# Kernel optimization log

Hardware: AMD Instinct MI355X
Metric: run time of the kernel (lower is better)

The kernel has to match this reference:

```python
import jax, jax.numpy as jnp
import numpy as np

EPS = 1e-6
D_CONV = 4

def _layernorm(x):
    m = jnp.mean(x, axis=-1, keepdims=True)
    v = jnp.mean((x - m) ** 2, axis=-1, keepdims=True)
    return (x - m) / jnp.sqrt(v + EPS)

def setup_inputs() -> dict:
    key = jax.random.key(0)
    ks = jax.random.split(key, 20)
    B, L, D = 2, 4096, 1024
    Di = D          # expand = 1
    N = 16          # d_state
    R = 64          # dt_rank = ceil(D/16)
    H = 4 * D       # mlp hidden
    s = 0.02
    rn = lambda k, sh: s * jax.random.normal(k, sh, dtype=jnp.float32)
    x = jax.random.normal(ks[0], (B, L, D), dtype=jnp.float32)
    path = jax.random.permutation(ks[1], L).astype(jnp.int32)
    path_rev = jnp.argsort(path).astype(jnp.int32)
    A_log = jnp.log(jnp.tile(jnp.arange(1, N + 1, dtype=jnp.float32)[None, :], (Di, 1)))
    return {
        'x': x, 'path': path, 'path_rev': path_rev,
        'in_proj_w': rn(ks[2], (2 * Di, D)),
        'conv_w': rn(ks[3], (Di, D_CONV)), 'conv_b': rn(ks[4], (Di,)),
        'x_proj_w': rn(ks[5], (R + 2 * N, Di)),
        'dt_proj_w': rn(ks[6], (Di, R)), 'dt_proj_b': rn(ks[7], (Di,)),
        'A_log': A_log, 'D_param': jnp.ones((Di,), dtype=jnp.float32),
        'out_proj_w': rn(ks[8], (D, Di)),
        'fc1_w': rn(ks[9], (H, D)), 'fc1_b': jnp.zeros((H,), dtype=jnp.float32),
        'fc2_w': rn(ks[10], (D, H)), 'fc2_b': jnp.zeros((D,), dtype=jnp.float32),
    }

def _mamba(u, in_proj_w, conv_w, conv_b, x_proj_w, dt_proj_w, dt_proj_b, A_log, D_param, out_proj_w):
    B, L, _ = u.shape
    N = A_log.shape[1]
    R = dt_proj_w.shape[1]
    xz = u @ in_proj_w.T                      # (B,L,2*Di)
    xi, z = jnp.split(xz, 2, axis=-1)
    # causal depthwise conv1d, kernel 4
    xpad = jnp.pad(xi, ((0, 0), (D_CONV - 1, 0), (0, 0)))
    xc = conv_b + sum(conv_w[:, k] * xpad[:, k:k + L, :] for k in range(D_CONV))
    xc = jax.nn.silu(xc)                      # (B,L,Di)
    proj = xc @ x_proj_w.T                    # (B,L,R+2N)
    dt_r = proj[..., :R]
    Bm = proj[..., R:R + N]                   # (B,L,N)
    Cm = proj[..., R + N:]                    # (B,L,N)
    dt = jax.nn.softplus(dt_r @ dt_proj_w.T + dt_proj_b)  # (B,L,Di)
    A = -jnp.exp(A_log)                       # (Di,N)

    def step(h, inp):
        dt_t, B_t, C_t, x_t = inp             # (B,Di),(B,N),(B,N),(B,Di)
        dA = jnp.exp(dt_t[:, :, None] * A)    # (B,Di,N)
        h = dA * h + (dt_t * x_t)[:, :, None] * B_t[:, None, :]
        y = jnp.einsum('bdn,bn->bd', h, C_t)
        return h, y

    h0 = jnp.zeros((B, xc.shape[-1], N), dtype=u.dtype)
    xs = (dt.transpose(1, 0, 2), Bm.transpose(1, 0, 2), Cm.transpose(1, 0, 2), xc.transpose(1, 0, 2))
    _, ys = jax.lax.scan(step, h0, xs)        # (L,B,Di)
    y = ys.transpose(1, 0, 2) + D_param * xc
    y = y * jax.nn.silu(z)
    return y @ out_proj_w.T

def reference(x, path, path_rev, in_proj_w, conv_w, conv_b, x_proj_w, dt_proj_w, dt_proj_b,
              A_log, D_param, out_proj_w, fc1_w, fc1_b, fc2_w, fc2_b):
    tmp1 = x[:, path, :]                      # zigzag gather
    tmp1 = _mamba(_layernorm(tmp1), in_proj_w, conv_w, conv_b, x_proj_w,
                  dt_proj_w, dt_proj_b, A_log, D_param, out_proj_w)
    x = x + tmp1[:, path_rev, :]              # zigzag scatter (inverse gather)
    h = _layernorm(x)
    h = jax.nn.gelu(h @ fc1_w.T + fc1_b, approximate=True) @ fc2_w.T + fc2_b
    return x + h
```

## Files before the change

### kernel.cpp

```cpp
#include <hip/hip_runtime.h>
#include <cstdint>
#include <cstddef>

typedef unsigned short u16;
typedef __bf16 bf16x8 __attribute__((ext_vector_type(8)));
typedef float f32x4 __attribute__((ext_vector_type(4)));

#define B_ 2
#define L_ 4096
#define D_ 1024
#define N_ 16
#define BL_ 8192
#define NC_ 64
#define LC_ 64

__device__ __forceinline__ float bf2f(u16 h) {
  union { unsigned int u; float f; } v; v.u = ((unsigned int)h) << 16; return v.f;
}
__device__ __forceinline__ u16 f2bf(float f) {
  union { float f; unsigned int u; } v; v.f = f;
  unsigned int r = v.u + 0x7FFFu + ((v.u >> 16) & 1u);
  return (u16)(r >> 16);
}
__device__ __forceinline__ float sigmoidf_(float x) { return 1.0f / (1.0f + __expf(-x)); }

#define WBF_TOT 11730944
__global__ __launch_bounds__(256) void cvt_w_k(
    const float* __restrict__ s0, const float* __restrict__ s1,
    const float* __restrict__ s2, const float* __restrict__ s3,
    const float* __restrict__ s4, const float* __restrict__ s5,
    u16* __restrict__ dst)
{
  int i = blockIdx.x * 256 + threadIdx.x;
  if (i >= WBF_TOT) return;
  float v;
  if (i < 2097152) v = s0[i];
  else if (i < 2228224) { int j = i - 2097152; v = (j < 98304) ? s1[j] : 0.0f; }
  else if (i < 2293760) v = s2[i - 2228224];
  else if (i < 3342336) v = s3[i - 2293760];
  else if (i < 7536640) v = s4[i - 3342336];
  else v = s5[i - 7536640];
  dst[i] = f2bf(v);
}

#define BM 128
#define BN 128
#define BK 32

enum { M_NONE = 0, M_PROJ = 1, M_SOFTPLUS = 2, M_GELU = 3, M_BIASRES = 4 };

template<int MODE>
__global__ __launch_bounds__(256) void gemm_bt(
    const u16* __restrict__ A, const u16* __restrict__ W,
    float* __restrict__ C, u16* __restrict__ C2,
    const float* __restrict__ bias, const float* __restrict__ resid,
    int M, int N, int K)
{
  __shared__ __align__(16) u16 As[BM * BK];
  __shared__ __align__(16) u16 Bs[BN * BK];
  const int bm = blockIdx.y * BM;
  const int bn = blockIdx.x * BN;
  const int tid = threadIdx.x;
  const int lane = tid & 63;
  const int wave = tid >> 6;
  const int wr = (wave >> 1) * 64;
  const int wc = (wave & 1) * 64;

  f32x4 acc[4][4];
#pragma unroll
  for (int i = 0; i < 4; ++i)
#pragma unroll
    for (int j = 0; j < 4; ++j)
#pragma unroll
      for (int r = 0; r < 4; ++r) acc[i][j][r] = 0.0f;

  const int r0 = tid >> 2;
  const int r1 = (tid + 256) >> 2;
  const int ke = (tid & 3) << 3;

  for (int k0 = 0; k0 < K; k0 += BK) {
    __builtin_amdgcn_global_load_lds(
        (const __attribute__((address_space(1))) void*)(A + (size_t)(bm + r0) * K + k0 + ke),
        (__attribute__((address_space(3))) void*)(&As[(size_t)tid * 8]), 16, 0, 0);
    __builtin_amdgcn_global_load_lds(
        (const __attribute__((address_space(1))) void*)(A + (size_t)(bm + r1) * K + k0 + ke),
        (__attribute__((address_space(3))) void*)(&As[(size_t)(tid + 256) * 8]), 16, 0, 0);
    __builtin_amdgcn_global_load_lds(
        (const __attribute__((address_space(1))) void*)(W + (size_t)(bn + r0) * K + k0 + ke),
        (__attribute__((address_space(3))) void*)(&Bs[(size_t)tid * 8]), 16, 0, 0);
    __builtin_amdgcn_global_load_lds(
        (const __attribute__((address_space(1))) void*)(W + (size_t)(bn + r1) * K + k0 + ke),
        (__attribute__((address_space(3))) void*)(&Bs[(size_t)(tid + 256) * 8]), 16, 0, 0);
    __syncthreads();
    const int kq = (lane >> 4) << 3;
    const int mr = lane & 15;
    bf16x8 af[4], bfr[4];
#pragma unroll
    for (int i = 0; i < 4; ++i)
      af[i] = *(const bf16x8*)(&As[(wr + i * 16 + mr) * BK + kq]);
#pragma unroll
    for (int j = 0; j < 4; ++j)
      bfr[j] = *(const bf16x8*)(&Bs[(wc + j * 16 + mr) * BK + kq]);
#pragma unroll
    for (int i = 0; i < 4; ++i)
#pragma unroll
      for (int j = 0; j < 4; ++j)
        acc[i][j] = __builtin_amdgcn_mfma_f32_16x16x32_bf16(af[i], bfr[j], acc[i][j], 0, 0, 0);
    __syncthreads();
  }

  const int mlo = (lane >> 4) << 2;
  const int nlo = lane & 15;
#pragma unroll
  for (int i = 0; i < 4; ++i) {
#pragma unroll
    for (int j = 0; j < 4; ++j) {
      int col = bn + wc + j * 16 + nlo;
      if (col < N) {
#pragma unroll
        for (int r = 0; r < 4; ++r) {
          int row = bm + wr + i * 16 + mlo + r;
          float v = acc[i][j][r];
          if constexpr (MODE == M_NONE) {
            C[(size_t)row * N + col] = v;
          } else if constexpr (MODE == M_PROJ) {
            C[(size_t)row * N + col] = v;
            if (col < 64) C2[((size_t)row << 6) + col] = f2bf(v);
          } else if constexpr (MODE == M_SOFTPLUS) {
            v += bias[col];
            C[(size_t)row * N + col] = (v > 20.0f) ? v : log1pf(__expf(v));
          } else if constexpr (MODE == M_GELU) {
            v += bias[col];
            float a = 0.7978845608028654f * (v + 0.044715f * v * v * v);
            float t = 1.0f - 2.0f / (__expf(2.0f * a) + 1.0f);
            C2[(size_t)row * N + col] = f2bf(0.5f * v * (1.0f + t));
          } else if constexpr (MODE == M_BIASRES) {
            C[(size_t)row * N + col] = v + bias[col] + resid[(size_t)row * N + col];
          }
        }
      }
    }
  }
}

__device__ __forceinline__ void blockReduce2(float& s, float& q) {
#pragma unroll
  for (int o = 32; o > 0; o >>= 1) { s += __shfl_down(s, o, 64); q += __shfl_down(q, o, 64); }
  __shared__ float red[2][4];
  int lane = threadIdx.x & 63, wave = threadIdx.x >> 6;
  if (lane == 0) { red[0][wave] = s; red[1][wave] = q; }
  __syncthreads();
  s = red[0][0] + red[0][1] + red[0][2] + red[0][3];
  q = red[1][0] + red[1][1] + red[1][2] + red[1][3];
}

__global__ __launch_bounds__(256) void ln_gather_k(
    const float* __restrict__ x, const int* __restrict__ path, u16* __restrict__ out)
{
  int b = blockIdx.x >> 12;
  int l = blockIdx.x & 4095;
  int src = path[l];
  const float* row = x + (((size_t)b * L_ + src) << 10);
  u16* orow = out + (((size_t)b * L_ + l) << 10);
  float v[4], s = 0.f, q = 0.f;
#pragma unroll
  for (int i = 0; i < 4; ++i) {
    v[i] = row[threadIdx.x + (i << 8)];
    s += v[i]; q += v[i] * v[i];
  }
  blockReduce2(s, q);
  float mean = s * (1.0f / 1024.0f);
  float var = q * (1.0f / 1024.0f) - mean * mean;
  float rstd = rsqrtf(var + 1e-6f);
#pragma unroll
  for (int i = 0; i < 4; ++i)
    orow[threadIdx.x + (i << 8)] = f2bf((v[i] - mean) * rstd);
}

__global__ __launch_bounds__(256) void ln_scatter_k(
    const float* __restrict__ x, const int* __restrict__ prev,
    const float* __restrict__ mo, float* __restrict__ xnew, u16* __restrict__ lnout)
{
  int b = blockIdx.x >> 12;
  int l = blockIdx.x & 4095;
  int pl = prev[l];
  const float* xr = x + (((size_t)b * L_ + l) << 10);
  const float* mr_ = mo + (((size_t)b * L_ + pl) << 10);
  size_t base = ((size_t)blockIdx.x) << 10;
  float v[4], s = 0.f, q = 0.f;
#pragma unroll
  for (int i = 0; i < 4; ++i) {
    v[i] = xr[threadIdx.x + (i << 8)] + mr_[threadIdx.x + (i << 8)];
    s += v[i]; q += v[i] * v[i];
  }
  blockReduce2(s, q);
  float mean = s * (1.0f / 1024.0f);
  float var = q * (1.0f / 1024.0f) - mean * mean;
  float rstd = rsqrtf(var + 1e-6f);
#pragma unroll
  for (int i = 0; i < 4; ++i) {
    xnew[base + threadIdx.x + (i << 8)] = v[i];
    lnout[base + threadIdx.x + (i << 8)] = f2bf((v[i] - mean) * rstd);
  }
}

__global__ __launch_bounds__(256) void conv_silu_k(
    const float* __restrict__ xz, const float* __restrict__ cw, const float* __restrict__ cb,
    u16* __restrict__ xc)
{
  int idx = blockIdx.x * 256 + threadIdx.x;
  int d = idx & 1023;
  int l = (idx >> 10) & 4095;
  int b = idx >> 22;
  float acc = cb[d];
#pragma unroll
  for (int k = 0; k < 4; ++k) {
    int ls = l + k - 3;
    if (ls >= 0)
      acc += cw[(d << 2) + k] * xz[(((size_t)b * L_ + ls) << 11) + d];
  }
  acc = acc * sigmoidf_(acc);
  xc[idx] = f2bf(acc);
}

__global__ __launch_bounds__(256) void scan_p1_k(
    const float* __restrict__ dt, const u16* __restrict__ xc, const float* __restrict__ proj,
    const float* __restrict__ A_log, float* __restrict__ acum, float* __restrict__ hloc)
{
  int c = blockIdx.x & (NC_ - 1);
  int q = (blockIdx.x >> 6) & 3;
  int b = blockIdx.x >> 8;
  int d = (q << 8) + threadIdx.x;
  float Arow[N_];
#pragma unroll
  for (int n = 0; n < N_; ++n) Arow[n] = -__expf(A_log[(d << 4) + n]);
  float h[N_], ac[N_];
#pragma unroll
  for (int n = 0; n < N_; ++n) { h[n] = 0.0f; ac[n] = 1.0f; }
  int l0 = c << 6;
  for (int i = 0; i < LC_; ++i) {
    size_t rowb = (size_t)b * L_ + (l0 + i);
    float dtv = dt[(rowb << 10) + d];
    float xv = bf2f(xc[(rowb << 10) + d]);
    float dtx = dtv * xv;
    const float* Bp = proj + rowb * 96 + 64;
#pragma unroll
    for (int n = 0; n < N_; ++n) {
      float dA = __expf(dtv * Arow[n]);
      h[n] = dA * h[n] + dtx * Bp[n];
      ac[n] *= dA;
    }
  }
  size_t sb = ((((size_t)b << 10) + d) << 10) + (c << 4);
#pragma unroll
  for (int n = 0; n < N_; ++n) { acum[sb + n] = ac[n]; hloc[sb + n] = h[n]; }
}

__global__ __launch_bounds__(256) void scan_p2_k(
    const float* __restrict__ acum, const float* __restrict__ hloc, float* __restrict__ hin)
{
  int idx = blockIdx.x * 256 + threadIdx.x;
  int n = idx & 15;
  int dn = idx >> 4;
  size_t base = ((size_t)dn << 10) + n;
  float hs = 0.0f;
  for (int c = 0; c < NC_; ++c) {
    hin[base + (c << 4)] = hs;
    hs = acum[base + (c << 4)] * hs + hloc[base + (c << 4)];
  }
}

__global__ __launch_bounds__(256) void scan_p3_k(
    const float* __restrict__ dt, const u16* __restrict__ xc, const float* __restrict__ proj,
    const float* __restrict__ A_log, const float* __restrict__ Dp, const float* __restrict__ hin,
    const float* __restrict__ xz, u16* __restrict__ yg)
{
  int c = blockIdx.x & (NC_ - 1);
  int q = (blockIdx.x >> 6) & 3;
  int b = blockIdx.x >> 8;
  int d = (q << 8) + threadIdx.x;
  float Arow[N_];
#pragma unroll
  for (int n = 0; n < N_; ++n) Arow[n] = -__expf(A_log[(d << 4) + n]);
  float h[N_];
  size_t sb = ((((size_t)b << 10) + d) << 10) + (c << 4);
#pragma unroll
  for (int n = 0; n < N_; ++n) h[n] = hin[sb + n];
  float Dv = Dp[d];
  int l0 = c << 6;
  for (int i = 0; i < LC_; ++i) {
    size_t rowb = (size_t)b * L_ + (l0 + i);
    float dtv = dt[(rowb << 10) + d];
    float xv = bf2f(xc[(rowb << 10) + d]);
    float dtx = dtv * xv;
    const float* Bp = proj + rowb * 96 + 64;
    const float* Cp = proj + rowb * 96 + 80;
    float y = 0.0f;
#pragma unroll
    for (int n = 0; n < N_; ++n) {
      float dA = __expf(dtv * Arow[n]);
      h[n] = dA * h[n] + dtx * Bp[n];
      y += h[n] * Cp[n];
    }
    y += Dv * xv;
    float zv = xz[(rowb << 11) + 1024 + d];
    yg[(rowb << 10) + d] = f2bf(y * zv * sigmoidf_(zv));
  }
}

extern "C" void kernel_launch(void* const* d_in, const int* in_sizes, int n_in,
                              void* d_out, int out_size, void* d_ws, size_t ws_size,
                              hipStream_t stream)
{
  const float* x_in      = (const float*)d_in[0];
  const int*   path      = (const int*)d_in[1];
  const int*   path_rev  = (const int*)d_in[2];
  const float* in_proj_w = (const float*)d_in[3];
  const float* conv_w    = (const float*)d_in[4];
  const float* conv_b    = (const float*)d_in[5];
  const float* x_proj_w  = (const float*)d_in[6];
  const float* dt_proj_w = (const float*)d_in[7];
  const float* dt_proj_b = (const float*)d_in[8];
  const float* A_log     = (const float*)d_in[9];
  const float* Dp        = (const float*)d_in[10];
  const float* out_pw    = (const float*)d_in[11];
  const float* fc1_w     = (const float*)d_in[12];
  const float* fc1_b     = (const float*)d_in[13];
  const float* fc2_w     = (const float*)d_in[14];
  const float* fc2_b     = (const float*)d_in[15];
  float* out = (float*)d_out;

  char* w = (char*)d_ws;
  size_t off = 0;
  auto alloc = [&](size_t bytes) -> char* {
    char* p = w + off;
    off = (off + bytes + 255) & ~(size_t)255;
    return p;
  };
  u16*   wbf   = (u16*)  alloc((size_t)WBF_TOT * 2);
  u16*   ln_bf = (u16*)  alloc((size_t)BL_ * 1024 * 2);
  float* xz    = (float*)alloc((size_t)BL_ * 2048 * 4);
  u16*   xc    = (u16*)  alloc((size_t)BL_ * 1024 * 2);
  char*  pool0 = alloc(0);
  float* proj  = (float*)alloc((size_t)BL_ * 96 * 4);
  u16*   dtr   = (u16*)  alloc((size_t)BL_ * 64 * 2);
  float* dt    = (float*)alloc((size_t)BL_ * 1024 * 4);
  float* acum  = (float*)alloc((size_t)2 * 1024 * NC_ * 16 * 4);
  float* hloc  = (float*)alloc((size_t)2 * 1024 * NC_ * 16 * 4);
  float* hin   = (float*)alloc((size_t)2 * 1024 * NC_ * 16 * 4);
  u16*   yg    = (u16*)  alloc((size_t)BL_ * 1024 * 2);
  float* mo    = xz;
  float* xnew  = (float*)((char*)xz + (size_t)BL_ * 1024 * 4);
  u16*   h1b   = (u16*)pool0;

  const u16* w_inp = wbf;
  const u16* w_xp  = wbf + 2097152;
  const u16* w_dtp = wbf + 2228224;
  const u16* w_op  = wbf + 2293760;
  const u16* w_fc1 = wbf + 3342336;
  const u16* w_fc2 = wbf + 7536640;

  dim3 blk(256);
  cvt_w_k<<<WBF_TOT / 256, blk, 0, stream>>>(in_proj_w, x_proj_w, dt_proj_w, out_pw,
                                             fc1_w, fc2_w, wbf);
  ln_gather_k<<<BL_, blk, 0, stream>>>(x_in, path, ln_bf);
  gemm_bt<M_NONE><<<dim3(16, 64), blk, 0, stream>>>(ln_bf, w_inp, xz, nullptr, nullptr, nullptr, 8192, 2048, 1024);
  conv_silu_k<<<(BL_ * 1024) / 256, blk, 0, stream>>>(xz, conv_w, conv_b, xc);
  gemm_bt<M_PROJ><<<dim3(1, 64), blk, 0, stream>>>(xc, w_xp, proj, dtr, nullptr, nullptr, 8192, 96, 1024);
  gemm_bt<M_SOFTPLUS><<<dim3(8, 64), blk, 0, stream>>>(dtr, w_dtp, dt, nullptr, dt_proj_b, nullptr, 8192, 1024, 64);
  scan_p1_k<<<2 * 4 * NC_, blk, 0, stream>>>(dt, xc, proj, A_log, acum, hloc);
  scan_p2_k<<<(2 * 1024 * 16) / 256, blk, 0, stream>>>(acum, hloc, hin);
  scan_p3_k<<<2 * 4 * NC_, blk, 0, stream>>>(dt, xc, proj, A_log, Dp, hin, xz, yg);
  gemm_bt<M_NONE><<<dim3(8, 64), blk, 0, stream>>>(yg, w_op, mo, nullptr, nullptr, nullptr, 8192, 1024, 1024);
  ln_scatter_k<<<BL_, blk, 0, stream>>>(x_in, path_rev, mo, xnew, ln_bf);
  gemm_bt<M_GELU><<<dim3(32, 64), blk, 0, stream>>>(ln_bf, w_fc1, nullptr, h1b, fc1_b, nullptr, 8192, 4096, 1024);
  gemm_bt<M_BIASRES><<<dim3(8, 64), blk, 0, stream>>>(h1b, w_fc2, out, nullptr, fc2_b, xnew, 8192, 1024, 4096);
}
```

Measured before the change: 682.1 us.

## Double-buffer GEMM LDS tiles, remap blocks per XCD, store xz/mo in bf16

The GEMM now double-buffers its A/B LDS tiles, issuing the next k-slice's global-to-LDS loads before computing the current one. This drops one barrier per iteration and overlaps load latency with MFMA work. Block IDs are remapped so each XCD handles a contiguous band of M rows, aiming for better L2 reuse. The in_proj and out_proj outputs (xz and mo) are written as bf16 instead of fp32, halving that traffic at some cost in precision; xnew gets its own allocation.

```diff
diff --git a/kernel.cpp b/kernel.cpp
--- a/kernel.cpp
+++ b/kernel.cpp
@@ -47,7 +47,11 @@
 #define BN 128
 #define BK 32
 
-enum { M_NONE = 0, M_PROJ = 1, M_SOFTPLUS = 2, M_GELU = 3, M_BIASRES = 4 };
+enum { M_BF16 = 0, M_PROJ = 1, M_SOFTPLUS = 2, M_GELU = 3, M_BIASRES = 4 };
+
+#define GLDS(gp, lp) __builtin_amdgcn_global_load_lds( \
+    (const __attribute__((address_space(1))) void*)(gp), \
+    (__attribute__((address_space(3))) void*)(lp), 16, 0, 0)
 
 template<int MODE>
 __global__ __launch_bounds__(256) void gemm_bt(
@@ -56,10 +60,18 @@
     const float* __restrict__ bias, const float* __restrict__ resid,
     int M, int N, int K)
 {
-  __shared__ __align__(16) u16 As[BM * BK];
-  __shared__ __align__(16) u16 Bs[BN * BK];
-  const int bm = blockIdx.y * BM;
-  const int bn = blockIdx.x * BN;
+  __shared__ __align__(16) u16 As[2][BM * BK];
+  __shared__ __align__(16) u16 Bs[2][BN * BK];
+
+  const int id = blockIdx.x + gridDim.x * blockIdx.y;
+  const int xcd = id & 7;
+  const int q = id >> 3;
+  const int bandH = gridDim.y >> 3;
+  const int xs = q % gridDim.x;
+  const int ys = xcd * bandH + q / gridDim.x;
+  const int bm = ys * BM;
+  const int bn = xs * BN;
+
   const int tid = threadIdx.x;
   const int lane = tid & 63;
   const int wave = tid >> 6;
@@ -75,38 +87,38 @@
       for (int r = 0; r < 4; ++r) acc[i][j][r] = 0.0f;
 
   const int r0 = tid >> 2;
-  const int r1 = (tid + 256) >> 2;
   const int ke = (tid & 3) << 3;
-
+  const u16* Ab = A + (size_t)(bm + r0) * K + ke;
+  const u16* Wb = W + (size_t)(bn + r0) * K + ke;
+  const size_t rstep = (size_t)64 * K;
+
+  auto issue = [&](int buf, int k0) {
+    GLDS(Ab + k0, &As[buf][tid * 8]);
+    GLDS(Ab + k0 + rstep, &As[buf][(tid + 256) * 8]);
+    GLDS(Wb + k0, &Bs[buf][tid * 8]);
+    GLDS(Wb + k0 + rstep, &Bs[buf][(tid + 256) * 8]);
+  };
+
+  issue(0, 0);
+  int cur = 0;
+  const int kq = (lane >> 4) << 3;
+  const int mr = lane & 15;
   for (int k0 = 0; k0 < K; k0 += BK) {
-    __builtin_amdgcn_global_load_lds(
-        (const __attribute__((address_space(1))) void*)(A + (size_t)(bm + r0) * K + k0 + ke),
-        (__attribute__((address_space(3))) void*)(&As[(size_t)tid * 8]), 16, 0, 0);
-    __builtin_amdgcn_global_load_lds(
-        (const __attribute__((address_space(1))) void*)(A + (size_t)(bm + r1) * K + k0 + ke),
-        (__attribute__((address_space(3))) void*)(&As[(size_t)(tid + 256) * 8]), 16, 0, 0);
-    __builtin_amdgcn_global_load_lds(
-        (const __attribute__((address_space(1))) void*)(W + (size_t)(bn + r0) * K + k0 + ke),
-        (__attribute__((address_space(3))) void*)(&Bs[(size_t)tid * 8]), 16, 0, 0);
-    __builtin_amdgcn_global_load_lds(
-        (const __attribute__((address_space(1))) void*)(W + (size_t)(bn + r1) * K + k0 + ke),
-        (__attribute__((address_space(3))) void*)(&Bs[(size_t)(tid + 256) * 8]), 16, 0, 0);
     __syncthreads();
-    const int kq = (lane >> 4) << 3;
-    const int mr = lane & 15;
+    if (k0 + BK < K) issue(cur ^ 1, k0 + BK);
     bf16x8 af[4], bfr[4];
 #pragma unroll
     for (int i = 0; i < 4; ++i)
-      af[i] = *(const bf16x8*)(&As[(wr + i * 16 + mr) * BK + kq]);
+      af[i] = *(const bf16x8*)(&As[cur][(wr + i * 16 + mr) * BK + kq]);
 #pragma unroll
     for (int j = 0; j < 4; ++j)
-      bfr[j] = *(const bf16x8*)(&Bs[(wc + j * 16 + mr) * BK + kq]);
+      bfr[j] = *(const bf16x8*)(&Bs[cur][(wc + j * 16 + mr) * BK + kq]);
 #pragma unroll
     for (int i = 0; i < 4; ++i)
 #pragma unroll
       for (int j = 0; j < 4; ++j)
         acc[i][j] = __builtin_amdgcn_mfma_f32_16x16x32_bf16(af[i], bfr[j], acc[i][j], 0, 0, 0);
-    __syncthreads();
+    cur ^= 1;
   }
 
   const int mlo = (lane >> 4) << 2;
@@ -121,10 +133,10 @@
         for (int r = 0; r < 4; ++r) {
           int row = bm + wr + i * 16 + mlo + r;
           float v = acc[i][j][r];
-          if constexpr (MODE == M_NONE) {
-            C[(size_t)row * N + col] = v;
+          if constexpr (MODE == M_BF16) {
+            C2[(size_t)row * N + col] = f2bf(v);
           } else if constexpr (MODE == M_PROJ) {
-            C[(size_t)row * N + col] = v;
+            C[(size_t)row * 96 + col] = v;
             if (col < 64) C2[((size_t)row << 6) + col] = f2bf(v);
           } else if constexpr (MODE == M_SOFTPLUS) {
             v += bias[col];
@@ -179,18 +191,18 @@
 
 __global__ __launch_bounds__(256) void ln_scatter_k(
     const float* __restrict__ x, const int* __restrict__ prev,
-    const float* __restrict__ mo, float* __restrict__ xnew, u16* __restrict__ lnout)
+    const u16* __restrict__ mo, float* __restrict__ xnew, u16* __restrict__ lnout)
 {
   int b = blockIdx.x >> 12;
   int l = blockIdx.x & 4095;
   int pl = prev[l];
   const float* xr = x + (((size_t)b * L_ + l) << 10);
-  const float* mr_ = mo + (((size_t)b * L_ + pl) << 10);
+  const u16* mr_ = mo + (((size_t)b * L_ + pl) << 10);
   size_t base = ((size_t)blockIdx.x) << 10;
   float v[4], s = 0.f, q = 0.f;
 #pragma unroll
   for (int i = 0; i < 4; ++i) {
-    v[i] = xr[threadIdx.x + (i << 8)] + mr_[threadIdx.x + (i << 8)];
+    v[i] = xr[threadIdx.x + (i << 8)] + bf2f(mr_[threadIdx.x + (i << 8)]);
     s += v[i]; q += v[i] * v[i];
   }
   blockReduce2(s, q);
@@ -205,7 +217,7 @@
 }
 
 __global__ __launch_bounds__(256) void conv_silu_k(
-    const float* __restrict__ xz, const float* __restrict__ cw, const float* __restrict__ cb,
+    const u16* __restrict__ xz, const float* __restrict__ cw, const float* __restrict__ cb,
     u16* __restrict__ xc)
 {
   int idx = blockIdx.x * 256 + threadIdx.x;
@@ -217,7 +229,7 @@
   for (int k = 0; k < 4; ++k) {
     int ls = l + k - 3;
     if (ls >= 0)
-      acc += cw[(d << 2) + k] * xz[(((size_t)b * L_ + ls) << 11) + d];
+      acc += cw[(d << 2) + k] * bf2f(xz[(((size_t)b * L_ + ls) << 11) + d]);
   }
   acc = acc * sigmoidf_(acc);
   xc[idx] = f2bf(acc);
@@ -273,7 +285,7 @@
 __global__ __launch_bounds__(256) void scan_p3_k(
     const float* __restrict__ dt, const u16* __restrict__ xc, const float* __restrict__ proj,
     const float* __restrict__ A_log, const float* __restrict__ Dp, const float* __restrict__ hin,
-    const float* __restrict__ xz, u16* __restrict__ yg)
+    const u16* __restrict__ xz, u16* __restrict__ yg)
 {
   int c = blockIdx.x & (NC_ - 1);
   int q = (blockIdx.x >> 6) & 3;
@@ -303,7 +315,7 @@
       y += h[n] * Cp[n];
     }
     y += Dv * xv;
-    float zv = xz[(rowb << 11) + 1024 + d];
+    float zv = bf2f(xz[(rowb << 11) + 1024 + d]);
     yg[(rowb << 10) + d] = f2bf(y * zv * sigmoidf_(zv));
   }
 }
@@ -339,7 +351,7 @@
   };
   u16*   wbf   = (u16*)  alloc((size_t)WBF_TOT * 2);
   u16*   ln_bf = (u16*)  alloc((size_t)BL_ * 1024 * 2);
-  float* xz    = (float*)alloc((size_t)BL_ * 2048 * 4);
+  u16*   xz    = (u16*)  alloc((size_t)BL_ * 2048 * 2);
   u16*   xc    = (u16*)  alloc((size_t)BL_ * 1024 * 2);
   char*  pool0 = alloc(0);
   float* proj  = (float*)alloc((size_t)BL_ * 96 * 4);
@@ -349,8 +361,8 @@
   float* hloc  = (float*)alloc((size_t)2 * 1024 * NC_ * 16 * 4);
   float* hin   = (float*)alloc((size_t)2 * 1024 * NC_ * 16 * 4);
   u16*   yg    = (u16*)  alloc((size_t)BL_ * 1024 * 2);
-  float* mo    = xz;
-  float* xnew  = (float*)((char*)xz + (size_t)BL_ * 1024 * 4);
+  float* xnew  = (float*)alloc((size_t)BL_ * 1024 * 4);
+  u16*   mo    = xz;
   u16*   h1b   = (u16*)pool0;
 
   const u16* w_inp = wbf;
@@ -364,14 +376,14 @@
   cvt_w_k<<<WBF_TOT / 256, blk, 0, stream>>>(in_proj_w, x_proj_w, dt_proj_w, out_pw,
                                              fc1_w, fc2_w, wbf);
   ln_gather_k<<<BL_, blk, 0, stream>>>(x_in, path, ln_bf);
-  gemm_bt<M_NONE><<<dim3(16, 64), blk, 0, stream>>>(ln_bf, w_inp, xz, nullptr, nullptr, nullptr, 8192, 2048, 1024);
+  gemm_bt<M_BF16><<<dim3(16, 64), blk, 0, stream>>>(ln_bf, w_inp, nullptr, xz, nullptr, nullptr, 8192, 2048, 1024);
   conv_silu_k<<<(BL_ * 1024) / 256, blk, 0, stream>>>(xz, conv_w, conv_b, xc);
   gemm_bt<M_PROJ><<<dim3(1, 64), blk, 0, stream>>>(xc, w_xp, proj, dtr, nullptr, nullptr, 8192, 96, 1024);
   gemm_bt<M_SOFTPLUS><<<dim3(8, 64), blk, 0, stream>>>(dtr, w_dtp, dt, nullptr, dt_proj_b, nullptr, 8192, 1024, 64);
   scan_p1_k<<<2 * 4 * NC_, blk, 0, stream>>>(dt, xc, proj, A_log, acum, hloc);
   scan_p2_k<<<(2 * 1024 * 16) / 256, blk, 0, stream>>>(acum, hloc, hin);
   scan_p3_k<<<2 * 4 * NC_, blk, 0, stream>>>(dt, xc, proj, A_log, Dp, hin, xz, yg);
-  gemm_bt<M_NONE><<<dim3(8, 64), blk, 0, stream>>>(yg, w_op, mo, nullptr, nullptr, nullptr, 8192, 1024, 1024);
+  gemm_bt<M_BF16><<<dim3(8, 64), blk, 0, stream>>>(yg, w_op, nullptr, mo, nullptr, nullptr, 8192, 1024, 1024);
   ln_scatter_k<<<BL_, blk, 0, stream>>>(x_in, path_rev, mo, xnew, ln_bf);
   gemm_bt<M_GELU><<<dim3(32, 64), blk, 0, stream>>>(ln_bf, w_fc1, nullptr, h1b, fc1_b, nullptr, 8192, 4096, 1024);
   gemm_bt<M_BIASRES><<<dim3(8, 64), blk, 0, stream>>>(h1b, w_fc2, out, nullptr, fc2_b, xnew, 8192, 1024, 4096);
```

Measured after the change: 638.2 us. -6.4%, faster.
